# Kernel tuning notes

Measured on AMD Instinct MI355X. Metric: run time of the kernel, lower is better.

## Reference

```python
import jax, jax.numpy as jnp
import numpy as np

N_NODES = 100000
N_EDGES = 3200000
N_FEAT = 128
N_GRAPHS = 1024
N_CLASSES = 10
K = 30  # global_sort_pool k


def setup_inputs() -> dict:
    key = jax.random.key(0)
    ks = jax.random.split(key, 20)
    p = lambda k, shape: jax.random.normal(k, shape, jnp.float32) * 0.1
    return {
        "x": jax.random.normal(ks[0], (N_NODES, N_FEAT), jnp.float32),
        "w1": p(ks[1], (N_FEAT, 32)), "b1": p(ks[2], (32,)),
        "w2": p(ks[3], (32, 32)),     "b2": p(ks[4], (32,)),
        "w3": p(ks[5], (32, 32)),     "b3": p(ks[6], (32,)),
        "w4": p(ks[7], (32, 1)),      "b4": p(ks[8], (1,)),
        "conv5_w": p(ks[9], (16, 1, 97)),  "conv5_b": p(ks[10], (16,)),
        "conv6_w": p(ks[11], (32, 16, 5)), "conv6_b": p(ks[12], (32,)),
        "fc1_w": p(ks[13], (352, 128)),    "fc1_b": p(ks[14], (128,)),
        "fc2_w": p(ks[15], (128, N_CLASSES)), "fc2_b": p(ks[16], (N_CLASSES,)),
        "edge_src": jax.random.randint(ks[17], (N_EDGES,), 0, N_NODES),
        "edge_dst": jax.random.randint(ks[18], (N_EDGES,), 0, N_NODES),
        "batch": jnp.sort(jax.random.randint(ks[19], (N_NODES,), 0, N_GRAPHS)),
        "num_graphs": N_GRAPHS,
    }


def _gcn_forward(x, w1, b1, w2, b2, w3, b3, w4, b4,
                 conv5_w, conv5_b, conv6_w, conv6_b,
                 fc1_w, fc1_b, fc2_w, fc2_b,
                 edge_src, edge_dst, batch, num_graphs):
    n = x.shape[0]
    # remove_self_loops: mask self-loop edges to weight 0 (shapes stay static)
    ew = (edge_src != edge_dst).astype(x.dtype)
    # gcn_norm with added self-loops (weight 1): deg includes self-loop
    deg = jax.ops.segment_sum(ew, edge_dst, num_segments=n) + 1.0
    dis = jax.lax.rsqrt(deg)                       # deg^{-1/2}
    enorm = dis[edge_src] * dis[edge_dst] * ew     # [E]
    snorm = (dis * dis)[:, None]                   # self-loop norm [n,1]

    def gcn_conv(h, W, b):
        h = h @ W                                   # [n, out]
        agg = jax.ops.segment_sum(h[edge_src] * enorm[:, None], edge_dst,
                                  num_segments=n) + h * snorm
        return agg + b

    x1 = jnp.tanh(gcn_conv(x,  w1, b1))   # [n,32]
    x2 = jnp.tanh(gcn_conv(x1, w2, b2))   # [n,32]
    x3 = jnp.tanh(gcn_conv(x2, w3, b3))   # [n,32]
    x4 = jnp.tanh(gcn_conv(x3, w4, b4))   # [n,1]
    xc = jnp.concatenate([x1, x2, x3, x4], axis=-1)  # [n,97]

    # global_sort_pool(k=K): per-graph sort by last channel, descending
    key_last = xc[:, -1]
    order = jnp.lexsort((-key_last, batch))          # primary: batch, secondary: desc key
    bs = batch[order]                                # sorted graph ids
    counts = jax.ops.segment_sum(jnp.ones_like(batch, jnp.int32), batch,
                                 num_segments=num_graphs)
    starts = jnp.cumsum(counts) - counts             # exclusive prefix sum
    rank = jnp.arange(n) - starts[bs]                # rank within own graph
    r = jnp.where(rank < K, rank, K)                 # overflow -> dummy slot K
    pooled = jnp.zeros((num_graphs, K + 1, 97), xc.dtype)
    pooled = pooled.at[bs, r].set(xc[order])
    pooled = pooled[:, :K, :].reshape(num_graphs, 1, K * 97)  # [B,1,2910]

    # Conv1d(1,16,97,97) + relu
    h = jax.lax.conv_general_dilated(pooled, conv5_w, (97,), 'VALID',
                                     dimension_numbers=('NCH', 'OIH', 'NCH'))
    h = jax.nn.relu(h + conv5_b[None, :, None])      # [B,16,30]
    # MaxPool1d(2,2)
    h = jax.lax.reduce_window(h, -jnp.inf, jax.lax.max,
                              (1, 1, 2), (1, 1, 2), 'VALID')  # [B,16,15]
    # Conv1d(16,32,5,1) + relu
    h = jax.lax.conv_general_dilated(h, conv6_w, (1,), 'VALID',
                                     dimension_numbers=('NCH', 'OIH', 'NCH'))
    h = jax.nn.relu(h + conv6_b[None, :, None])      # [B,32,11]
    h = h.reshape(num_graphs, -1)                    # [B,352]

    h = jax.nn.relu(h @ fc1_w + fc1_b)               # [B,128]; dropout = identity (eval)
    return jax.nn.log_softmax(h @ fc2_w + fc2_b, axis=-1)  # [B,num_classes]


def reference(x, w1, b1, w2, b2, w3, b3, w4, b4,
              conv5_w, conv5_b, conv6_w, conv6_b,
              fc1_w, fc1_b, fc2_w, fc2_b,
              edge_src, edge_dst, batch, num_graphs):
    return _gcn_forward(x, w1, b1, w2, b2, w3, b3, w4, b4,
                        conv5_w, conv5_b, conv6_w, conv6_b,
                        fc1_w, fc1_b, fc2_w, fc2_b,
                        edge_src, edge_dst, batch, num_graphs)
```

## Files before the change

kernel.cpp:

```cpp
#include <hip/hip_runtime.h>
#include <hip/hip_bf16.h>

#define N_NODES 100000
#define N_EDGES 3200000
#define NGRAPH 1024
#define KTOP 30
#define PELEM (NGRAPH * KTOP * 97)

#define NBKT 782
#define NTILE 391
#define TILE 8192
#define BKT_CAP 4736

typedef __hip_bfloat16 bf16;

__device__ __forceinline__ float u2f(unsigned short h) {
    return __uint_as_float(((unsigned int)h) << 16);
}
__device__ __forceinline__ float LD(const void* p, int i, int bf) {
    if (bf) return u2f(((const unsigned short*)p)[i]);
    return ((const float*)p)[i];
}

__global__ void k_detect(const void* w1, int* flag) {
    if (threadIdx.x == 0 && blockIdx.x == 0) {
        const unsigned short* u = (const unsigned short*)w1;
        int plausible = 0;
        for (int i = 0; i < 64; i++) {
            float a = fabsf(u2f(u[2 * i]));
            if (a == 0.f || (a >= 9.765625e-4f && a <= 2.0f)) plausible++;
        }
        *flag = (plausible >= 40) ? 1 : 0;
    }
}

__global__ void k_icur(int* __restrict__ cur) {
    int i = blockIdx.x * 256 + threadIdx.x;
    if (i < NBKT) cur[i] = i * BKT_CAP;
}

__global__ __launch_bounds__(256) void k_scat(const int* __restrict__ src,
                                              const int* __restrict__ dst,
                                              int* __restrict__ cur,
                                              int* __restrict__ ebuf) {
    __shared__ int pk[TILE];
    __shared__ unsigned short bk[TILE];
    __shared__ int h[NBKT];
    __shared__ int base[NBKT];
    int tid = threadIdx.x;
    int ebase = blockIdx.x * TILE;
    for (int i = tid; i < NBKT; i += 256) h[i] = 0;
    __syncthreads();
    for (int i = tid; i < TILE; i += 256) {
        int e = ebase + i;
        int bkt = 0xFFFF;
        if (e < N_EDGES) {
            int s = __builtin_nontemporal_load(src + e);
            int d = __builtin_nontemporal_load(dst + e);
            if (s != d) {
                bkt = d >> 7;
                pk[i] = ((d & 127) << 17) | s;
                atomicAdd(&h[bkt], 1);
            }
        }
        bk[i] = (unsigned short)bkt;
    }
    __syncthreads();
    for (int i = tid; i < NBKT; i += 256) {
        int c = h[i];
        base[i] = c ? atomicAdd(&cur[i], c) : 0;
    }
    __syncthreads();
    for (int i = tid; i < NBKT; i += 256) h[i] = 0;
    __syncthreads();
    for (int i = tid; i < TILE; i += 256) {
        int bkt = bk[i];
        if (bkt != 0xFFFF) {
            int p = base[bkt] + atomicAdd(&h[bkt], 1);
            if (p < (bkt + 1) * BKT_CAP) ebuf[p] = pk[i];
        }
    }
}

__global__ __launch_bounds__(256) void k_bcsr(const int* __restrict__ ebuf,
                                              const int* __restrict__ cur,
                                              int* __restrict__ rs,
                                              int* __restrict__ re,
                                              float* __restrict__ dis,
                                              int* __restrict__ csr) {
    __shared__ int dloc[128];
    __shared__ int sc[128];
    int b = blockIdx.x;
    int node0 = b << 7;
    int nn = N_NODES - node0; if (nn > 128) nn = 128;
    int tid = threadIdx.x;
    if (tid < 128) dloc[tid] = 0;
    __syncthreads();
    int s = b * BKT_CAP;
    int cnt = cur[b] - s; if (cnt > BKT_CAP) cnt = BKT_CAP;
    int e = s + cnt;
    for (int i = s + tid; i < e; i += 256)
        atomicAdd(&dloc[ebuf[i] >> 17], 1);
    __syncthreads();
    if (tid < 128) sc[tid] = dloc[tid];
    __syncthreads();
    for (int off = 1; off < 128; off <<= 1) {
        int t = (tid >= off && tid < 128) ? sc[tid - off] : 0;
        __syncthreads();
        if (tid < 128) sc[tid] += t;
        __syncthreads();
    }
    if (tid < nn) {
        int st = s + sc[tid] - dloc[tid];
        rs[node0 + tid] = st;
        re[node0 + tid] = st + dloc[tid];
        dis[node0 + tid] = rsqrtf((float)dloc[tid] + 1.0f);
    }
    __syncthreads();
    if (tid < 128) dloc[tid] = s + sc[tid] - dloc[tid];
    __syncthreads();
    for (int i = s + tid; i < e; i += 256) {
        int pv = ebuf[i];
        int pos = atomicAdd(&dloc[pv >> 17], 1);
        csr[pos] = pv & 0x1FFFF;
    }
}

__global__ void k_gstart(const int* __restrict__ batch, int* __restrict__ gstart) {
    int g = blockIdx.x * 256 + threadIdx.x;
    if (g > NGRAPH) return;
    int lo = 0, hi = N_NODES;
    while (lo < hi) {
        int mid = (lo + hi) >> 1;
        if (batch[mid] < g) lo = mid + 1; else hi = mid;
    }
    gstart[g] = lo;
}

__global__ __launch_bounds__(256) void k_mm1(const void* __restrict__ x,
                                             const void* __restrict__ w,
                                             const int* __restrict__ flagp,
                                             const float* __restrict__ dis,
                                             float* __restrict__ ts) {
    __shared__ float Wl[128 * 32];
    __shared__ float Xs[32][128];
    int bf = *flagp;
    int tid = threadIdx.x;
    int nbase = blockIdx.x * 32;
    if (bf) {
        const ushort4* wv = (const ushort4*)w;
        for (int idx = tid; idx < 1024; idx += 256) {
            ushort4 h = wv[idx];
            int p = idx * 4;
            Wl[p] = u2f(h.x); Wl[p + 1] = u2f(h.y); Wl[p + 2] = u2f(h.z); Wl[p + 3] = u2f(h.w);
        }
        const ushort4* xv = (const ushort4*)x;
        for (int idx = tid; idx < 1024; idx += 256) {
            int nd = idx >> 5, q = idx & 31;
            ushort4 h = xv[(size_t)(nbase + nd) * 32 + q];
            float* d = &Xs[nd][q * 4];
            d[0] = u2f(h.x); d[1] = u2f(h.y); d[2] = u2f(h.z); d[3] = u2f(h.w);
        }
    } else {
        const float* wf = (const float*)w;
        for (int idx = tid; idx < 4096; idx += 256) Wl[idx] = wf[idx];
        const float* xf = (const float*)x;
        for (int idx = tid; idx < 4096; idx += 256)
            Xs[idx >> 7][idx & 127] = xf[(size_t)nbase * 128 + idx];
    }
    __syncthreads();
    int grp = tid >> 5, col = tid & 31;
    for (int rep = 0; rep < 4; rep++) {
        int sub = grp + 8 * rep;
        int node = nbase + sub;
        float acc = 0.f;
#pragma unroll 8
        for (int k = 0; k < 128; k++) acc += Xs[sub][k] * Wl[k * 32 + col];
        ts[node * 32 + col] = dis[node] * acc;
    }
}

__global__ __launch_bounds__(256) void k_agg(const float4* __restrict__ ts,
                                             const int* __restrict__ rs,
                                             const int* __restrict__ re,
                                             const int* __restrict__ csr,
                                             const float* __restrict__ dis,
                                             const void* __restrict__ b,
                                             const int* __restrict__ flagp,
                                             float4* __restrict__ out) {
    int node = blockIdx.x * 4 + (threadIdx.x >> 6);
    int lane = threadIdx.x & 63;
    int q   = lane & 7;
    int grp = lane >> 3;
    int bf = *flagp;
    int s = rs[node], e = re[node];
    float4 a0 = make_float4(0.f, 0.f, 0.f, 0.f);
    float4 a1 = a0, a2 = a0, a3 = a0;
    int i = s + grp;
    for (; i + 24 < e; i += 32) {
        int v0 = csr[i], v1 = csr[i + 8], v2 = csr[i + 16], v3 = csr[i + 24];
        float4 m0 = ts[v0 * 8 + q];
        float4 m1 = ts[v1 * 8 + q];
        float4 m2 = ts[v2 * 8 + q];
        float4 m3 = ts[v3 * 8 + q];
        a0.x += m0.x; a0.y += m0.y; a0.z += m0.z; a0.w += m0.w;
        a1.x += m1.x; a1.y += m1.y; a1.z += m1.z; a1.w += m1.w;
        a2.x += m2.x; a2.y += m2.y; a2.z += m2.z; a2.w += m2.w;
        a3.x += m3.x; a3.y += m3.y; a3.z += m3.z; a3.w += m3.w;
    }
    for (; i < e; i += 8) {
        float4 m = ts[csr[i] * 8 + q];
        a0.x += m.x; a0.y += m.y; a0.z += m.z; a0.w += m.w;
    }
    float4 acc;
    acc.x = (a0.x + a1.x) + (a2.x + a3.x);
    acc.y = (a0.y + a1.y) + (a2.y + a3.y);
    acc.z = (a0.z + a1.z) + (a2.z + a3.z);
    acc.w = (a0.w + a1.w) + (a2.w + a3.w);
#pragma unroll
    for (int off = 8; off < 64; off <<= 1) {
        acc.x += __shfl_xor(acc.x, off);
        acc.y += __shfl_xor(acc.y, off);
        acc.z += __shfl_xor(acc.z, off);
        acc.w += __shfl_xor(acc.w, off);
    }
    if (grp == 0) {
        float4 self = ts[node * 8 + q];
        float d = dis[node];
        float4 r;
        r.x = tanhf(d * (acc.x + self.x) + LD(b, q * 4 + 0, bf));
        r.y = tanhf(d * (acc.y + self.y) + LD(b, q * 4 + 1, bf));
        r.z = tanhf(d * (acc.z + self.z) + LD(b, q * 4 + 2, bf));
        r.w = tanhf(d * (acc.w + self.w) + LD(b, q * 4 + 3, bf));
        out[node * 8 + q] = r;
    }
}

template<int DO_TS4>
__global__ __launch_bounds__(256) void k_aggz(const float4* __restrict__ xin,
                                              const int* __restrict__ rs,
                                              const int* __restrict__ re,
                                              const int* __restrict__ csr,
                                              const float* __restrict__ dis,
                                              const void* __restrict__ W,
                                              const void* __restrict__ b,
                                              const void* __restrict__ w4,
                                              const int* __restrict__ flagp,
                                              float* __restrict__ xout,
                                              float* __restrict__ ts4) {
    __shared__ float Wl[1024];
    __shared__ float W4l[32];
    __shared__ float Z[4][32];
    int tid = threadIdx.x;
    int bf = *flagp;
    if (bf) {
        ushort4 h = ((const ushort4*)W)[tid];
        int p = tid * 4;
        Wl[p] = u2f(h.x); Wl[p + 1] = u2f(h.y); Wl[p + 2] = u2f(h.z); Wl[p + 3] = u2f(h.w);
    } else {
        float4 v = ((const float4*)W)[tid];
        int p = tid * 4;
        Wl[p] = v.x; Wl[p + 1] = v.y; Wl[p + 2] = v.z; Wl[p + 3] = v.w;
    }
    if (DO_TS4 && tid < 32) W4l[tid] = LD(w4, tid, bf);

    int wid = tid >> 6;
    int node = blockIdx.x * 4 + wid;
    int lane = tid & 63;
    int q   = lane & 7;
    int grp = lane >> 3;
    int s = rs[node], e = re[node];
    float4 a0 = make_float4(0.f, 0.f, 0.f, 0.f);
    float4 a1 = a0, a2 = a0, a3 = a0;
    int i = s + grp;
    for (; i + 24 < e; i += 32) {
        int v0 = csr[i], v1 = csr[i + 8], v2 = csr[i + 16], v3 = csr[i + 24];
        float d0 = dis[v0], d1 = dis[v1], d2 = dis[v2], d3 = dis[v3];
        float4 m0 = xin[v0 * 8 + q];
        float4 m1 = xin[v1 * 8 + q];
        float4 m2 = xin[v2 * 8 + q];
        float4 m3 = xin[v3 * 8 + q];
        a0.x += d0 * m0.x; a0.y += d0 * m0.y; a0.z += d0 * m0.z; a0.w += d0 * m0.w;
        a1.x += d1 * m1.x; a1.y += d1 * m1.y; a1.z += d1 * m1.z; a1.w += d1 * m1.w;
        a2.x += d2 * m2.x; a2.y += d2 * m2.y; a2.z += d2 * m2.z; a2.w += d2 * m2.w;
        a3.x += d3 * m3.x; a3.y += d3 * m3.y; a3.z += d3 * m3.z; a3.w += d3 * m3.w;
    }
    for (; i < e; i += 8) {
        int v = csr[i];
        float dv = dis[v];
        float4 m = xin[v * 8 + q];
        a0.x += dv * m.x; a0.y += dv * m.y; a0.z += dv * m.z; a0.w += dv * m.w;
    }
    float4 acc;
    acc.x = (a0.x + a1.x) + (a2.x + a3.x);
    acc.y = (a0.y + a1.y) + (a2.y + a3.y);
    acc.z = (a0.z + a1.z) + (a2.z + a3.z);
    acc.w = (a0.w + a1.w) + (a2.w + a3.w);
#pragma unroll
    for (int off = 8; off < 64; off <<= 1) {
        acc.x += __shfl_xor(acc.x, off);
        acc.y += __shfl_xor(acc.y, off);
        acc.z += __shfl_xor(acc.z, off);
        acc.w += __shfl_xor(acc.w, off);
    }
    if (grp == 0) {
        float4 self = xin[node * 8 + q];
        float di = dis[node];
        Z[wid][q * 4 + 0] = acc.x + di * self.x;
        Z[wid][q * 4 + 1] = acc.y + di * self.y;
        Z[wid][q * 4 + 2] = acc.z + di * self.z;
        Z[wid][q * 4 + 3] = acc.w + di * self.w;
    }
    __syncthreads();
    int nd = tid >> 6;
    int col = tid & 31;
    int kbase = (tid & 32) >> 1;
    const float* zr = Z[nd];
    float a = 0.f;
#pragma unroll
    for (int k2 = 0; k2 < 16; k2++) a += zr[kbase + k2] * Wl[(kbase + k2) * 32 + col];
    a += __shfl_xor(a, 32);
    int n2 = blockIdx.x * 4 + nd;
    float di2 = dis[n2];
    float xo = tanhf(di2 * a + LD(b, col, bf));
    if (!(tid & 32)) xout[n2 * 32 + col] = xo;
    if (DO_TS4) {
        float t4 = xo * W4l[col];
#pragma unroll
        for (int off = 1; off < 32; off <<= 1) t4 += __shfl_xor(t4, off);
        if ((tid & 63) == 0) ts4[n2] = di2 * t4;
    }
}

__global__ __launch_bounds__(256) void k_agg1(const float* __restrict__ ts4,
                                              const int* __restrict__ rs,
                                              const int* __restrict__ re,
                                              const int* __restrict__ csr,
                                              const float* __restrict__ dis,
                                              const void* __restrict__ b4,
                                              const int* __restrict__ flagp,
                                              float* __restrict__ x4) {
    int node = blockIdx.x * 16 + (threadIdx.x >> 4);
    int lane = threadIdx.x & 15;
    int s = rs[node], e = re[node];
    float acc = 0.f;
    for (int i = s + lane; i < e; i += 16) acc += ts4[csr[i]];
#pragma unroll
    for (int off = 1; off < 16; off <<= 1) acc += __shfl_xor(acc, off);
    if (lane == 0) {
        int bf = *flagp;
        x4[node] = tanhf(dis[node] * (acc + ts4[node]) + LD(b4, 0, bf));
    }
}

__global__ __launch_bounds__(256) void k_rank(const int* __restrict__ batch,
                                              const int* __restrict__ gstart,
                                              const float* __restrict__ x4,
                                              int* __restrict__ sel) {
    int i = blockIdx.x * 256 + threadIdx.x;
    if (i >= N_NODES) return;
    int g = batch[i];
    int s = gstart[g], e = gstart[g + 1];
    float ki = x4[i];
    int rank = 0;
    for (int j = s; j < e; j++) {
        float kj = x4[j];
        rank += (kj > ki) || (kj == ki && j < i);
    }
    if (rank < KTOP) sel[g * KTOP + rank] = i;
}

__global__ __launch_bounds__(256) void k_pool(const float* __restrict__ x1,
                                              const float* __restrict__ x2,
                                              const float* __restrict__ x3,
                                              const float* __restrict__ x4,
                                              const int* __restrict__ sel,
                                              float* __restrict__ P) {
    int idx = blockIdx.x * 256 + threadIdx.x;
    if (idx >= PELEM) return;
    int g = idx / (KTOP * 97);
    int r = idx - g * (KTOP * 97);
    int p = r / 97;
    int f = r - p * 97;
    int v = sel[g * KTOP + p];
    float val = 0.f;
    if (v >= 0) {
        if (f < 32)      val = x1[v * 32 + f];
        else if (f < 64) val = x2[v * 32 + f - 32];
        else if (f < 96) val = x3[v * 32 + f - 64];
        else             val = x4[v];
    }
    P[idx] = val;
}

__global__ __launch_bounds__(256) void k_head(
    const float* __restrict__ Pg,
    const void* __restrict__ w5, const void* __restrict__ b5,
    const void* __restrict__ w6, const void* __restrict__ b6,
    const void* __restrict__ f1w, const void* __restrict__ f1b,
    const void* __restrict__ f2w, const void* __restrict__ f2b,
    const int* __restrict__ flagp, void* __restrict__ out) {
    __shared__ float P[KTOP * 97];
    __shared__ float W5[16 * 97];
    __shared__ float W6[32 * 16 * 5];
    __shared__ float H5[16][30];
    __shared__ float M[16][15];
    __shared__ float H6[352];
    __shared__ float Rp[256];
    __shared__ float R1[128];
    __shared__ float L[10];
    __shared__ float mls;
    int g = blockIdx.x;
    int tid = threadIdx.x;
    int bf = *flagp;

    for (int i = tid; i < KTOP * 97; i += 256) P[i] = Pg[g * (KTOP * 97) + i];
    if (bf) {
        const ushort4* w5v = (const ushort4*)w5;
        for (int i = tid; i < 388; i += 256) {
            ushort4 h = w5v[i];
            int p = i * 4;
            W5[p] = u2f(h.x); W5[p + 1] = u2f(h.y); W5[p + 2] = u2f(h.z); W5[p + 3] = u2f(h.w);
        }
        const ushort4* w6v = (const ushort4*)w6;
        for (int i = tid; i < 640; i += 256) {
            ushort4 h = w6v[i];
            int p = i * 4;
            W6[p] = u2f(h.x); W6[p + 1] = u2f(h.y); W6[p + 2] = u2f(h.z); W6[p + 3] = u2f(h.w);
        }
    } else {
        for (int i = tid; i < 16 * 97; i += 256) W5[i] = ((const float*)w5)[i];
        for (int i = tid; i < 2560; i += 256) W6[i] = ((const float*)w6)[i];
    }
    __syncthreads();
    for (int idx = tid; idx < 480; idx += 256) {
        int o = idx / 30, p = idx - o * 30;
        float acc = LD(b5, o, bf);
        const float* pr = &P[p * 97];
        const float* wr = &W5[o * 97];
        for (int f = 0; f < 97; f++) acc += wr[f] * pr[f];
        H5[o][p] = fmaxf(acc, 0.f);
    }
    __syncthreads();
    for (int idx = tid; idx < 240; idx += 256) {
        int o = idx / 15, q = idx - o * 15;
        M[o][q] = fmaxf(H5[o][2 * q], H5[o][2 * q + 1]);
    }
    __syncthreads();
    for (int idx = tid; idx < 352; idx += 256) {
        int oc = idx / 11, tp = idx - oc * 11;
        float acc = LD(b6, oc, bf);
        const float* wr = &W6[oc * 80];
        for (int ic = 0; ic < 16; ic++) {
#pragma unroll
            for (int k = 0; k < 5; k++)
                acc += wr[ic * 5 + k] * M[ic][tp + k];
        }
        H6[idx] = fmaxf(acc, 0.f);
    }
    __syncthreads();
    {
        int half = tid >> 7, col = tid & 127;
        int base = half * 176;
        float a = 0.f;
        for (int i = 0; i < 176; i++) {
            int ii = base + i;
            a += H6[ii] * LD(f1w, ii * 128 + col, bf);
        }
        Rp[tid] = a;
    }
    __syncthreads();
    if (tid < 128) R1[tid] = fmaxf(LD(f1b, tid, bf) + Rp[tid] + Rp[128 + tid], 0.f);
    __syncthreads();
    if (tid < 10) {
        float acc = LD(f2b, tid, bf);
        for (int k = 0; k < 128; k++) acc += R1[k] * LD(f2w, k * 10 + tid, bf);
        L[tid] = acc;
    }
    __syncthreads();
    if (tid == 0) {
        float m = L[0];
        for (int c = 1; c < 10; c++) m = fmaxf(m, L[c]);
        float ssum = 0.f;
        for (int c = 0; c < 10; c++) ssum += expf(L[c] - m);
        mls = m + logf(ssum);
    }
    __syncthreads();
    if (tid < 10) {
        float v = L[tid] - mls;
        if (bf) ((bf16*)out)[g * 10 + tid] = __float2bfloat16(v);
        else    ((float*)out)[g * 10 + tid] = v;
    }
}

extern "C" void kernel_launch(void* const* d_in, const int* in_sizes, int n_in,
                              void* d_out, int out_size, void* d_ws, size_t ws_size,
                              hipStream_t stream) {
    const void* x   = d_in[0];
    const void* w1  = d_in[1];  const void* b1  = d_in[2];
    const void* w2  = d_in[3];  const void* b2  = d_in[4];
    const void* w3  = d_in[5];  const void* b3  = d_in[6];
    const void* w4  = d_in[7];  const void* b4  = d_in[8];
    const void* w5  = d_in[9];  const void* b5  = d_in[10];
    const void* w6  = d_in[11]; const void* b6  = d_in[12];
    const void* f1w = d_in[13]; const void* f1b = d_in[14];
    const void* f2w = d_in[15]; const void* f2b = d_in[16];
    const int* esrc  = (const int*)d_in[17];
    const int* edst  = (const int*)d_in[18];
    const int* batch = (const int*)d_in[19];

    char* w = (char*)d_ws;
    size_t off = 0;
    auto alloc = [&](size_t bytes) {
        void* p = w + off;
        off += (bytes + 255) & ~(size_t)255;
        return p;
    };
    int*   flag   = (int*)  alloc(256);
    int*   rs     = (int*)  alloc((size_t)N_NODES * 4);
    int*   re     = (int*)  alloc((size_t)N_NODES * 4);
    float* dis    = (float*)alloc((size_t)N_NODES * 4);
    int*   csr    = (int*)  alloc((size_t)NBKT * BKT_CAP * 4);
    float* t      = (float*)alloc((size_t)N_NODES * 32 * 4);
    float* x1     = (float*)alloc((size_t)N_NODES * 32 * 4);
    float* x2     = (float*)alloc((size_t)N_NODES * 32 * 4);
    float* x3     = (float*)alloc((size_t)N_NODES * 32 * 4);
    float* x4     = (float*)alloc((size_t)N_NODES * 4);
    float* ts4b   = (float*)alloc((size_t)N_NODES * 4);
    int*   gstart = (int*)  alloc((size_t)(NGRAPH + 1) * 4);
    int*   sel    = (int*)  alloc((size_t)NGRAPH * KTOP * 4);
    float* Pg     = (float*)alloc((size_t)PELEM * 4);
    int*   cur    = (int*)  alloc((size_t)NBKT * 4);
    (void)ws_size; (void)n_in; (void)in_sizes; (void)out_size;

    int* ebuf = (int*)t;

    (void)hipMemsetAsync(sel, 0xFF, (size_t)NGRAPH * KTOP * 4, stream);

    int nb   = (N_NODES + 255) / 256;
    int mb32 = N_NODES / 32;
    int ab   = N_NODES / 4;
    int a1b  = N_NODES / 16;
    int pb   = (PELEM + 255) / 256;

    k_detect<<<1, 64, 0, stream>>>(w1, flag);
    k_icur<<<(NBKT + 255) / 256, 256, 0, stream>>>(cur);
    k_scat<<<NTILE, 256, 0, stream>>>(esrc, edst, cur, ebuf);
    k_bcsr<<<NBKT, 256, 0, stream>>>(ebuf, cur, rs, re, dis, csr);
    k_gstart<<<5, 256, 0, stream>>>(batch, gstart);

    k_mm1<<<mb32, 256, 0, stream>>>(x, w1, flag, dis, t);
    k_agg<<<ab, 256, 0, stream>>>((const float4*)t, rs, re, csr, dis, b1, flag, (float4*)x1);
    k_aggz<0><<<ab, 256, 0, stream>>>((const float4*)x1, rs, re, csr, dis, w2, b2, w4, flag, x2, ts4b);
    k_aggz<1><<<ab, 256, 0, stream>>>((const float4*)x2, rs, re, csr, dis, w3, b3, w4, flag, x3, ts4b);
    k_agg1<<<a1b, 256, 0, stream>>>(ts4b, rs, re, csr, dis, b4, flag, x4);
    k_rank<<<nb, 256, 0, stream>>>(batch, gstart, x4, sel);
    k_pool<<<pb, 256, 0, stream>>>(x1, x2, x3, x4, sel, Pg);
    k_head<<<NGRAPH, 256, 0, stream>>>(Pg, w5, b5, w6, b6,
                                       f1w, f1b, f2w, f2b, flag, (void*)d_out);
}
```

Before: 561.8 us.

## Pack source degree into CSR entries and register-tile the first matmul

```diff
diff --git a/kernel.cpp b/kernel.cpp
--- a/kernel.cpp
+++ b/kernel.cpp
@@ -13,6 +13,7 @@
 #define BKT_CAP 4736
 
 typedef __hip_bfloat16 bf16;
+typedef float vfloat4 __attribute__((ext_vector_type(4)));
 
 __device__ __forceinline__ float u2f(unsigned short h) {
     return __uint_as_float(((unsigned int)h) << 16);
@@ -82,12 +83,12 @@
     }
 }
 
-__global__ __launch_bounds__(256) void k_bcsr(const int* __restrict__ ebuf,
+__global__ __launch_bounds__(256) void k_bcnt(const int* __restrict__ ebuf,
                                               const int* __restrict__ cur,
                                               int* __restrict__ rs,
                                               int* __restrict__ re,
                                               float* __restrict__ dis,
-                                              int* __restrict__ csr) {
+                                              int* __restrict__ deg) {
     __shared__ int dloc[128];
     __shared__ int sc[128];
     int b = blockIdx.x;
@@ -115,14 +116,33 @@
         rs[node0 + tid] = st;
         re[node0 + tid] = st + dloc[tid];
         dis[node0 + tid] = rsqrtf((float)dloc[tid] + 1.0f);
-    }
-    __syncthreads();
-    if (tid < 128) dloc[tid] = s + sc[tid] - dloc[tid];
-    __syncthreads();
+        deg[node0 + tid] = dloc[tid];
+    }
+}
+
+__global__ __launch_bounds__(256) void k_bfill(const int* __restrict__ ebuf,
+                                               const int* __restrict__ cur,
+                                               const int* __restrict__ rs,
+                                               const int* __restrict__ deg,
+                                               int* __restrict__ csr) {
+    __shared__ int cl[128];
+    int b = blockIdx.x;
+    int node0 = b << 7;
+    int tid = threadIdx.x;
+    if (tid < 128) {
+        int n = node0 + tid;
+        cl[tid] = (n < N_NODES) ? rs[n] : 0;
+    }
+    __syncthreads();
+    int s = b * BKT_CAP;
+    int cnt = cur[b] - s; if (cnt > BKT_CAP) cnt = BKT_CAP;
+    int e = s + cnt;
     for (int i = s + tid; i < e; i += 256) {
         int pv = ebuf[i];
-        int pos = atomicAdd(&dloc[pv >> 17], 1);
-        csr[pos] = pv & 0x1FFFF;
+        int srcn = pv & 0x1FFFF;
+        int pos = atomicAdd(&cl[pv >> 17], 1);
+        int d = deg[srcn];
+        csr[pos] = (d << 17) | srcn;
     }
 }
 
@@ -137,47 +157,67 @@
     gstart[g] = lo;
 }
 
+#define MM1_B 64
 __global__ __launch_bounds__(256) void k_mm1(const void* __restrict__ x,
                                              const void* __restrict__ w,
                                              const int* __restrict__ flagp,
                                              const float* __restrict__ dis,
                                              float* __restrict__ ts) {
-    __shared__ float Wl[128 * 32];
-    __shared__ float Xs[32][128];
+    __shared__ float Xs[MM1_B][129];
+    __shared__ float Wf[128 * 32];
     int bf = *flagp;
     int tid = threadIdx.x;
-    int nbase = blockIdx.x * 32;
+    int nbase = blockIdx.x * MM1_B;
     if (bf) {
         const ushort4* wv = (const ushort4*)w;
         for (int idx = tid; idx < 1024; idx += 256) {
             ushort4 h = wv[idx];
             int p = idx * 4;
-            Wl[p] = u2f(h.x); Wl[p + 1] = u2f(h.y); Wl[p + 2] = u2f(h.z); Wl[p + 3] = u2f(h.w);
-        }
-        const ushort4* xv = (const ushort4*)x;
+            Wf[p] = u2f(h.x); Wf[p + 1] = u2f(h.y); Wf[p + 2] = u2f(h.z); Wf[p + 3] = u2f(h.w);
+        }
+        const unsigned short* xb = (const unsigned short*)x;
         for (int idx = tid; idx < 1024; idx += 256) {
-            int nd = idx >> 5, q = idx & 31;
-            ushort4 h = xv[(size_t)(nbase + nd) * 32 + q];
-            float* d = &Xs[nd][q * 4];
-            d[0] = u2f(h.x); d[1] = u2f(h.y); d[2] = u2f(h.z); d[3] = u2f(h.w);
+            int row = idx >> 4, c8 = (idx & 15) * 8;
+            int gn = nbase + row; if (gn >= N_NODES) gn = N_NODES - 1;
+            uint4 v = *(const uint4*)(xb + (size_t)gn * 128 + c8);
+            float* d = &Xs[row][c8];
+            d[0] = u2f((unsigned short)(v.x & 0xffff)); d[1] = u2f((unsigned short)(v.x >> 16));
+            d[2] = u2f((unsigned short)(v.y & 0xffff)); d[3] = u2f((unsigned short)(v.y >> 16));
+            d[4] = u2f((unsigned short)(v.z & 0xffff)); d[5] = u2f((unsigned short)(v.z >> 16));
+            d[6] = u2f((unsigned short)(v.w & 0xffff)); d[7] = u2f((unsigned short)(v.w >> 16));
         }
     } else {
         const float* wf = (const float*)w;
-        for (int idx = tid; idx < 4096; idx += 256) Wl[idx] = wf[idx];
-        const float* xf = (const float*)x;
-        for (int idx = tid; idx < 4096; idx += 256)
-            Xs[idx >> 7][idx & 127] = xf[(size_t)nbase * 128 + idx];
-    }
-    __syncthreads();
-    int grp = tid >> 5, col = tid & 31;
-    for (int rep = 0; rep < 4; rep++) {
-        int sub = grp + 8 * rep;
-        int node = nbase + sub;
-        float acc = 0.f;
-#pragma unroll 8
-        for (int k = 0; k < 128; k++) acc += Xs[sub][k] * Wl[k * 32 + col];
-        ts[node * 32 + col] = dis[node] * acc;
-    }
+        for (int idx = tid; idx < 4096; idx += 256) Wf[idx] = wf[idx];
+        const float4* xv = (const float4*)x;
+        for (int idx = tid; idx < 2048; idx += 256) {
+            int row = idx >> 5, c4 = (idx & 31) * 4;
+            int gn = nbase + row; if (gn >= N_NODES) gn = N_NODES - 1;
+            float4 v = xv[(size_t)gn * 32 + (c4 >> 2)];
+            float* d = &Xs[row][c4];
+            d[0] = v.x; d[1] = v.y; d[2] = v.z; d[3] = v.w;
+        }
+    }
+    __syncthreads();
+    int tn = (tid & 15) * 4;
+    int tc = (tid >> 4) * 2;
+    float a00 = 0.f, a01 = 0.f, a10 = 0.f, a11 = 0.f;
+    float a20 = 0.f, a21 = 0.f, a30 = 0.f, a31 = 0.f;
+#pragma unroll 4
+    for (int k = 0; k < 128; k++) {
+        float2 wv = *(const float2*)&Wf[k * 32 + tc];
+        float x0 = Xs[tn + 0][k], x1 = Xs[tn + 1][k];
+        float x2 = Xs[tn + 2][k], x3 = Xs[tn + 3][k];
+        a00 += x0 * wv.x; a01 += x0 * wv.y;
+        a10 += x1 * wv.x; a11 += x1 * wv.y;
+        a20 += x2 * wv.x; a21 += x2 * wv.y;
+        a30 += x3 * wv.x; a31 += x3 * wv.y;
+    }
+    int n0 = nbase + tn;
+    if (n0 + 0 < N_NODES) { float d = dis[n0 + 0]; *(float2*)&ts[(n0 + 0) * 32 + tc] = make_float2(d * a00, d * a01); }
+    if (n0 + 1 < N_NODES) { float d = dis[n0 + 1]; *(float2*)&ts[(n0 + 1) * 32 + tc] = make_float2(d * a10, d * a11); }
+    if (n0 + 2 < N_NODES) { float d = dis[n0 + 2]; *(float2*)&ts[(n0 + 2) * 32 + tc] = make_float2(d * a20, d * a21); }
+    if (n0 + 3 < N_NODES) { float d = dis[n0 + 3]; *(float2*)&ts[(n0 + 3) * 32 + tc] = make_float2(d * a30, d * a31); }
 }
 
 __global__ __launch_bounds__(256) void k_agg(const float4* __restrict__ ts,
@@ -198,7 +238,8 @@
     float4 a1 = a0, a2 = a0, a3 = a0;
     int i = s + grp;
     for (; i + 24 < e; i += 32) {
-        int v0 = csr[i], v1 = csr[i + 8], v2 = csr[i + 16], v3 = csr[i + 24];
+        int v0 = csr[i] & 0x1FFFF, v1 = csr[i + 8] & 0x1FFFF;
+        int v2 = csr[i + 16] & 0x1FFFF, v3 = csr[i + 24] & 0x1FFFF;
         float4 m0 = ts[v0 * 8 + q];
         float4 m1 = ts[v1 * 8 + q];
         float4 m2 = ts[v2 * 8 + q];
@@ -209,7 +250,7 @@
         a3.x += m3.x; a3.y += m3.y; a3.z += m3.z; a3.w += m3.w;
     }
     for (; i < e; i += 8) {
-        float4 m = ts[csr[i] * 8 + q];
+        float4 m = ts[(csr[i] & 0x1FFFF) * 8 + q];
         a0.x += m.x; a0.y += m.y; a0.z += m.z; a0.w += m.w;
     }
     float4 acc;
@@ -227,12 +268,12 @@
     if (grp == 0) {
         float4 self = ts[node * 8 + q];
         float d = dis[node];
-        float4 r;
+        vfloat4 r;
         r.x = tanhf(d * (acc.x + self.x) + LD(b, q * 4 + 0, bf));
         r.y = tanhf(d * (acc.y + self.y) + LD(b, q * 4 + 1, bf));
         r.z = tanhf(d * (acc.z + self.z) + LD(b, q * 4 + 2, bf));
         r.w = tanhf(d * (acc.w + self.w) + LD(b, q * 4 + 3, bf));
-        out[node * 8 + q] = r;
+        __builtin_nontemporal_store(r, (vfloat4*)&out[node * 8 + q]);
     }
 }
 
@@ -274,8 +315,12 @@
     float4 a1 = a0, a2 = a0, a3 = a0;
     int i = s + grp;
     for (; i + 24 < e; i += 32) {
-        int v0 = csr[i], v1 = csr[i + 8], v2 = csr[i + 16], v3 = csr[i + 24];
-        float d0 = dis[v0], d1 = dis[v1], d2 = dis[v2], d3 = dis[v3];
+        int p0 = csr[i], p1 = csr[i + 8], p2 = csr[i + 16], p3 = csr[i + 24];
+        int v0 = p0 & 0x1FFFF, v1 = p1 & 0x1FFFF, v2 = p2 & 0x1FFFF, v3 = p3 & 0x1FFFF;
+        float d0 = rsqrtf((float)(p0 >> 17) + 1.0f);
+        float d1 = rsqrtf((float)(p1 >> 17) + 1.0f);
+        float d2 = rsqrtf((float)(p2 >> 17) + 1.0f);
+        float d3 = rsqrtf((float)(p3 >> 17) + 1.0f);
         float4 m0 = xin[v0 * 8 + q];
         float4 m1 = xin[v1 * 8 + q];
         float4 m2 = xin[v2 * 8 + q];
@@ -286,8 +331,9 @@
         a3.x += d3 * m3.x; a3.y += d3 * m3.y; a3.z += d3 * m3.z; a3.w += d3 * m3.w;
     }
     for (; i < e; i += 8) {
-        int v = csr[i];
-        float dv = dis[v];
+        int pv = csr[i];
+        int v = pv & 0x1FFFF;
+        float dv = rsqrtf((float)(pv >> 17) + 1.0f);
         float4 m = xin[v * 8 + q];
         a0.x += dv * m.x; a0.y += dv * m.y; a0.z += dv * m.z; a0.w += dv * m.w;
     }
@@ -344,7 +390,7 @@
     int lane = threadIdx.x & 15;
     int s = rs[node], e = re[node];
     float acc = 0.f;
-    for (int i = s + lane; i < e; i += 16) acc += ts4[csr[i]];
+    for (int i = s + lane; i < e; i += 16) acc += ts4[csr[i] & 0x1FFFF];
 #pragma unroll
     for (int off = 1; off < 16; off <<= 1) acc += __shfl_xor(acc, off);
     if (lane == 0) {
@@ -520,6 +566,7 @@
     int*   rs     = (int*)  alloc((size_t)N_NODES * 4);
     int*   re     = (int*)  alloc((size_t)N_NODES * 4);
     float* dis    = (float*)alloc((size_t)N_NODES * 4);
+    int*   deg    = (int*)  alloc((size_t)N_NODES * 4);
     int*   csr    = (int*)  alloc((size_t)NBKT * BKT_CAP * 4);
     float* t      = (float*)alloc((size_t)N_NODES * 32 * 4);
     float* x1     = (float*)alloc((size_t)N_NODES * 32 * 4);
@@ -538,7 +585,7 @@
     (void)hipMemsetAsync(sel, 0xFF, (size_t)NGRAPH * KTOP * 4, stream);
 
     int nb   = (N_NODES + 255) / 256;
-    int mb32 = N_NODES / 32;
+    int mb64 = (N_NODES + MM1_B - 1) / MM1_B;
     int ab   = N_NODES / 4;
     int a1b  = N_NODES / 16;
     int pb   = (PELEM + 255) / 256;
@@ -546,10 +593,11 @@
     k_detect<<<1, 64, 0, stream>>>(w1, flag);
     k_icur<<<(NBKT + 255) / 256, 256, 0, stream>>>(cur);
     k_scat<<<NTILE, 256, 0, stream>>>(esrc, edst, cur, ebuf);
-    k_bcsr<<<NBKT, 256, 0, stream>>>(ebuf, cur, rs, re, dis, csr);
+    k_bcnt<<<NBKT, 256, 0, stream>>>(ebuf, cur, rs, re, dis, deg);
+    k_bfill<<<NBKT, 256, 0, stream>>>(ebuf, cur, rs, deg, csr);
     k_gstart<<<5, 256, 0, stream>>>(batch, gstart);
 
-    k_mm1<<<mb32, 256, 0, stream>>>(x, w1, flag, dis, t);
+    k_mm1<<<mb64, 256, 0, stream>>>(x, w1, flag, dis, t);
     k_agg<<<ab, 256, 0, stream>>>((const float4*)t, rs, re, csr, dis, b1, flag, (float4*)x1);
     k_aggz<0><<<ab, 256, 0, stream>>>((const float4*)x1, rs, re, csr, dis, w2, b2, w4, flag, x2, ts4b);
     k_aggz<1><<<ab, 256, 0, stream>>>((const float4*)x2, rs, re, csr, dis, w3, b3, w4, flag, x3, ts4b);
```

Result: no change. 561.3 us (-0.1%).
